# Kernel optimization log

Hardware: AMD Instinct MI355X
Metric: run time of the kernel (lower is better)

Reference implementation:

```python
import jax, jax.numpy as jnp
import numpy as np

B, NP, NAA = 8, 2048, 512        # proteins, atoms, residues
K, K2 = 16, 14                   # spatial K-NN (K_atom), sequence K-NN (K_neighbor)
D_EMB, NG, F, F2, NCAT = 16, 64, 128, 128, 39
EPS = 1e-6

def _gather(x, idx):
    # x: [B, N, ...], idx: [B, ...] int -> x[b, idx[b]]
    return jax.vmap(lambda xb, ib: xb[ib])(x, idx)

def setup_inputs() -> dict:
    key = jax.random.key(0)
    ks = jax.random.split(key, 9)
    return dict(
        frame_indices=jax.random.randint(ks[0], (B, NP, 3), 0, NP, dtype=jnp.int32),
        attr_idx=jax.random.randint(ks[1], (B, NP), 0, NCAT, dtype=jnp.int32),
        seq_atom=jnp.sort(jax.random.randint(ks[2], (B, NP), 0, NAA, dtype=jnp.int32), axis=-1),
        seq_aa=jnp.broadcast_to(jnp.arange(NAA, dtype=jnp.int32), (B, NAA)),
        point_clouds=jax.random.normal(ks[3], (B, NP, 3), dtype=jnp.float32) * 10.0,
        mframe=jnp.ones((B, NP, 1), jnp.float32),
        mseq_aa=jnp.ones((B, NAA, 1), jnp.float32),
        embed_table=jax.random.normal(ks[4], (NCAT, D_EMB), dtype=jnp.float32) * 0.1,
        gauss_mu=jax.random.normal(ks[5], (NG, 3), dtype=jnp.float32) * 3.0,
        gauss_sigma=jnp.full((NG, 3), 2.0, jnp.float32),
        W_filter=jax.random.normal(ks[6], (NG, D_EMB, F), dtype=jnp.float32) / np.sqrt(NG * D_EMB).astype(np.float32),
        W_att=jax.random.normal(ks[7], (F, 1), dtype=jnp.float32) * 0.1,
        W_feat=jax.random.normal(ks[8], (F, F2), dtype=jnp.float32) / np.sqrt(F).astype(np.float32),
        bn_gamma=jnp.ones((F2,), jnp.float32),
        bn_beta=jnp.zeros((F2,), jnp.float32),
    )

def reference(frame_indices, attr_idx, seq_atom, seq_aa, point_clouds, mframe, mseq_aa,
              embed_table, gauss_mu, gauss_sigma, W_filter, W_att, W_feat, bn_gamma, bn_beta):
    # ---- Frame_Builder: orthonormal local frame per atom from index triplets ----
    pts = _gather(point_clouds, frame_indices)                    # [B,NP,3,3]
    center = pts[..., 0, :]
    u1 = pts[..., 1, :] - center
    u2 = pts[..., 2, :] - center
    e1 = u1 / (jnp.linalg.norm(u1, axis=-1, keepdims=True) + EPS)
    nrm = jnp.cross(u1, u2)
    e3 = nrm / (jnp.linalg.norm(nrm, axis=-1, keepdims=True) + EPS)
    e2 = jnp.cross(e3, e1)
    R = jnp.stack([e1, e2, e3], axis=-2)                          # [B,NP,3,3] rows = frame axes
    # ---- Neighborhood_Embedding: spatial K-NN + gaussian spatio-chemical filters ----
    d2 = jnp.sum((center[:, :, None, :] - center[:, None, :, :]) ** 2, axis=-1)   # [B,NP,NP]
    _, nbr = jax.lax.top_k(-d2, K)                                # [B,NP,K]
    delta = _gather(center, nbr) - center[:, :, None, :]          # [B,NP,K,3]
    local = jnp.einsum('bikd,bird->bikr', delta, R)               # neighbor coords in local frame
    inv_s2 = 1.0 / (gauss_sigma ** 2 + EPS)                       # [NG,3]
    q = (jnp.einsum('bikd,nd->bikn', local ** 2, inv_s2)
         - 2.0 * jnp.einsum('bikd,nd->bikn', local, gauss_mu * inv_s2)
         + jnp.sum(gauss_mu ** 2 * inv_s2, axis=-1))
    gauss = jnp.exp(-0.5 * q)                                     # [B,NP,K,NG]
    attr = embed_table[attr_idx] * mframe                         # [B,NP,D_EMB]
    attr_nbr = _gather(attr, nbr)                                 # [B,NP,K,D_EMB]
    Z = jnp.einsum('bikn,bikd->bind', gauss, attr_nbr)            # contract neighbors first
    y = jax.nn.relu(jnp.einsum('bind,ndf->bif', Z, W_filter)) * mframe   # [B,NP,F]
    att = (y @ W_att) * mframe                                    # [B,NP,1]
    feat = (y @ W_feat) * mframe                                  # [B,NP,F2]
    # ---- Neighborhood_Computation: K2 atoms nearest in sequence index per residue ----
    diff = jnp.abs(seq_aa[:, :, None] - seq_atom[:, None, :]).astype(jnp.float32)   # [B,NAA,NP]
    _, idx = jax.lax.top_k(-diff, K2)                             # [B,NAA,K2]
    att_l = _gather(att, idx)[..., 0]                             # [B,NAA,K2]
    feat_l = _gather(feat, idx)                                   # [B,NAA,K2,F2]
    diff_l = jnp.take_along_axis(diff, idx, axis=-1)
    gate = 1.0 - jnp.clip(diff_l, 0.0, 1.0)                       # pool_mask = 1 - index_distance
    # ---- Attention pooling over local atom neighborhood ----
    w = gate * jnp.exp(att_l - jnp.max(att_l, axis=-1, keepdims=True))
    w = w / (jnp.sum(w, axis=-1, keepdims=True) + EPS)
    pooled = jnp.einsum('bak,bakf->baf', w, feat_l) * mseq_aa     # [B,NAA,F2]
    # ---- MaskedBatchNorm1d + ReLU ----
    msum = jnp.sum(mseq_aa) + EPS
    mean = jnp.sum(pooled * mseq_aa, axis=(0, 1)) / msum
    var = jnp.sum(((pooled - mean) ** 2) * mseq_aa, axis=(0, 1)) / msum
    out = (pooled - mean) / jnp.sqrt(var + 1e-5) * bn_gamma + bn_beta
    out = jax.nn.relu(out) * mseq_aa
    return (out, mseq_aa)
```

## Files before the change

### kernel.cpp

```cpp
#include <hip/hip_runtime.h>
#include <math.h>

#define BB 8
#define NP 2048
#define NAA 512
#define KNN 16
#define KK2 14
#define DE 16
#define NG 64
#define FF 128
#define FF2 128
#define NCAT 39
#define EPSV 1e-6f

typedef __attribute__((ext_vector_type(8))) short bf16x8;
typedef __attribute__((ext_vector_type(4))) float f32x4;

__device__ __forceinline__ float bf16r(float x) {
    unsigned u = __float_as_uint(x);
    u = u + 0x7FFFu + ((u >> 16) & 1u);
    return __uint_as_float(u & 0xFFFF0000u);
}
__device__ __forceinline__ unsigned short bf16u(float x) {
    unsigned u = __float_as_uint(x);
    u = u + 0x7FFFu + ((u >> 16) & 1u);
    return (unsigned short)(u >> 16);
}

#define OFF_CENTER   0u
#define OFF_R        262144u
#define OFF_ATTR     1048576u
#define OFF_NBR      2097152u
#define OFF_ATT      3145728u
#define OFF_FEAT     3211264u
#define OFF_POOLED   11599872u
#define OFF_WFFRAG   (OFF_POOLED)
#define OFF_WFEATFRAG (OFF_POOLED + 262144u)
#define OFF_START    13697024u
#define OFF_PARTS    13713536u
#define OFF_PARTQ    13746304u
#define OFF_SS       13779072u

__global__ __launch_bounds__(256) void k_prep(
    const float* __restrict__ Wf, const float* __restrict__ Wfeat,
    unsigned short* __restrict__ WfF, unsigned short* __restrict__ WfeatF)
{
    int id = blockIdx.x * 256 + threadIdx.x;
    if (id < 32*8*64*8) {
        int i = id & 7, l = (id >> 3) & 63, nt = (id >> 9) & 7, s = id >> 12;
        int row = s*32 + (l >> 4)*8 + i;
        int col = nt*16 + (l & 15);
        WfF[id] = bf16u(Wf[(size_t)row*FF + col]);
    } else {
        int id2 = id - 32*8*64*8;
        if (id2 < 4*8*64*8) {
            int i = id2 & 7, l = (id2 >> 3) & 63, nt = (id2 >> 9) & 7, s = id2 >> 12;
            int row = s*32 + (l >> 4)*8 + i;
            int col = nt*16 + (l & 15);
            WfeatF[id2] = bf16u(Wfeat[(size_t)row*FF2 + col]);
        }
    }
}

__global__ __launch_bounds__(256) void k_frames(
    const int* __restrict__ fidx, const int* __restrict__ aidx,
    const float* __restrict__ pc, const float* __restrict__ mframe,
    const float* __restrict__ emb,
    float* __restrict__ center4, float* __restrict__ R12, float* __restrict__ attr16)
{
    int t = blockIdx.x * 256 + threadIdx.x;
    if (t >= BB * NP) return;
    int b = t / NP;
    const float* pcb = pc + (size_t)b * NP * 3;
    int i0 = fidx[t*3+0], i1 = fidx[t*3+1], i2 = fidx[t*3+2];
    float cx = pcb[i0*3+0], cy = pcb[i0*3+1], cz = pcb[i0*3+2];
    float ax = pcb[i1*3+0]-cx, ay = pcb[i1*3+1]-cy, az = pcb[i1*3+2]-cz;
    float bx = pcb[i2*3+0]-cx, by = pcb[i2*3+1]-cy, bz = pcb[i2*3+2]-cz;
    float n1 = sqrtf(ax*ax + ay*ay + az*az) + EPSV;
    float e1x = ax/n1, e1y = ay/n1, e1z = az/n1;
    float nx = ay*bz - az*by;
    float ny = az*bx - ax*bz;
    float nz = ax*by - ay*bx;
    float n3 = sqrtf(nx*nx + ny*ny + nz*nz) + EPSV;
    float e3x = nx/n3, e3y = ny/n3, e3z = nz/n3;
    float e2x = e3y*e1z - e3z*e1y;
    float e2y = e3z*e1x - e3x*e1z;
    float e2z = e3x*e1y - e3y*e1x;

    float4 c4; c4.x = cx; c4.y = cy; c4.z = cz; c4.w = 0.f;
    *(float4*)(center4 + (size_t)t*4) = c4;
    float* Rp = R12 + (size_t)t*12;
    Rp[0]=bf16r(e1x); Rp[1]=bf16r(e1y); Rp[2]=bf16r(e1z);
    Rp[3]=bf16r(e2x); Rp[4]=bf16r(e2y); Rp[5]=bf16r(e2z);
    Rp[6]=bf16r(e3x); Rp[7]=bf16r(e3y); Rp[8]=bf16r(e3z);

    int ai = aidx[t];
    float m = mframe[t];
    const float* er = emb + (size_t)ai * DE;
    float* ap = attr16 + (size_t)t * DE;
    #pragma unroll
    for (int d = 0; d < DE; ++d) ap[d] = bf16r(er[d] * m);
}

__global__ __launch_bounds__(256) void k_knn(
    const float* __restrict__ center4, int* __restrict__ nbr)
{
    __shared__ __align__(16) float sx[NP], sy[NP], sz[NP];
    __shared__ unsigned long long lists[16*126];
    __shared__ int cntS[16];
    __shared__ unsigned int TqU[16];
    unsigned int* kbufA = (unsigned int*)lists;

    int b = blockIdx.x >> 7;
    int qchunk = blockIdx.x & 127;
    int t = threadIdx.x;
    const float* cb = center4 + (size_t)b * NP * 4;
    for (int j = t; j < NP; j += 256) {
        float4 c = *(const float4*)(cb + (size_t)j*4);
        sx[j] = c.x; sy[j] = c.y; sz[j] = c.z;
    }
    __syncthreads();

    int qloc = t & 15, split = t >> 4;
    int q = qchunk * 16 + qloc;
    float qx = sx[q], qy = sy[q], qz = sz[q];
    int j0 = split * 128;
    int stag = split * 8;

    unsigned int e0a = ~0u, e1a = ~0u;
    unsigned int e0b = ~0u, e1b = ~0u;
    unsigned int e0c = ~0u, e1c = ~0u;
    unsigned int e0d = ~0u, e1d = ~0u;
    for (int jj = 0; jj < 128; jj += 4) {
        int j = j0 + ((jj + stag) & 127);
        float4 x4 = *(const float4*)(&sx[j]);
        float4 y4 = *(const float4*)(&sy[j]);
        float4 z4 = *(const float4*)(&sz[j]);
        float dx0 = __fsub_rn(qx, x4.x), dy0 = __fsub_rn(qy, y4.x), dz0 = __fsub_rn(qz, z4.x);
        float dx1 = __fsub_rn(qx, x4.y), dy1 = __fsub_rn(qy, y4.y), dz1 = __fsub_rn(qz, z4.y);
        float dx2 = __fsub_rn(qx, x4.z), dy2 = __fsub_rn(qy, y4.z), dz2 = __fsub_rn(qz, z4.z);
        float dx3 = __fsub_rn(qx, x4.w), dy3 = __fsub_rn(qy, y4.w), dz3 = __fsub_rn(qz, z4.w);
        unsigned c0 = __float_as_uint(__fadd_rn(__fadd_rn(__fmul_rn(dx0,dx0), __fmul_rn(dy0,dy0)), __fmul_rn(dz0,dz0)));
        unsigned c1 = __float_as_uint(__fadd_rn(__fadd_rn(__fmul_rn(dx1,dx1), __fmul_rn(dy1,dy1)), __fmul_rn(dz1,dz1)));
        unsigned c2 = __float_as_uint(__fadd_rn(__fadd_rn(__fmul_rn(dx2,dx2), __fmul_rn(dy2,dy2)), __fmul_rn(dz2,dz2)));
        unsigned c3 = __float_as_uint(__fadd_rn(__fadd_rn(__fmul_rn(dx3,dx3), __fmul_rn(dy3,dy3)), __fmul_rn(dz3,dz3)));
        unsigned n1;
        n1 = max(e0a, min(e1a, c0)); e0a = min(e0a, c0); e1a = n1;
        n1 = max(e0b, min(e1b, c1)); e0b = min(e0b, c1); e1b = n1;
        n1 = max(e0c, min(e1c, c2)); e0c = min(e0c, c2); e1c = n1;
        n1 = max(e0d, min(e1d, c3)); e0d = min(e0d, c3); e1d = n1;
    }
    kbufA[0*256 + t] = e0a;
    kbufA[1*256 + t] = e1a;
    kbufA[2*256 + t] = e0b;
    kbufA[3*256 + t] = e1b;
    kbufA[4*256 + t] = e0c;
    kbufA[5*256 + t] = e1c;
    kbufA[6*256 + t] = e0d;
    kbufA[7*256 + t] = e1d;
    __syncthreads();

    if (t < 16) {
        unsigned int arr[16];
        #pragma unroll
        for (int s = 0; s < 16; ++s) arr[s] = ~0u;
        for (int sp = 0; sp < 16; ++sp) {
            int lidx = sp*16 + t;
            #pragma unroll
            for (int ch = 0; ch < 4; ++ch) {
                #pragma unroll
                for (int s = 0; s < 2; ++s) {
                    unsigned int v = kbufA[(ch*2 + s)*256 + lidx];
                    if (v >= arr[15]) break;
                    unsigned int c = v;
                    #pragma unroll
                    for (int u = 0; u < 16; ++u) {
                        unsigned int lo = min(c, arr[u]), hi = max(c, arr[u]);
                        arr[u] = lo; c = hi;
                    }
                }
            }
        }
        TqU[t] = arr[15];
        cntS[t] = 0;
    }
    __syncthreads();
    unsigned int T = TqU[qloc];

    for (int jj = 0; jj < 128; jj += 4) {
        int j = j0 + ((jj + stag) & 127);
        float4 x4 = *(const float4*)(&sx[j]);
        float4 y4 = *(const float4*)(&sy[j]);
        float4 z4 = *(const float4*)(&sz[j]);
        #pragma unroll
        for (int c4i = 0; c4i < 4; ++c4i) {
            float xx = c4i==0?x4.x:c4i==1?x4.y:c4i==2?x4.z:x4.w;
            float yy = c4i==0?y4.x:c4i==1?y4.y:c4i==2?y4.z:y4.w;
            float zz = c4i==0?z4.x:c4i==1?z4.y:c4i==2?z4.z:z4.w;
            float dx = __fsub_rn(qx, xx);
            float dy = __fsub_rn(qy, yy);
            float dz = __fsub_rn(qz, zz);
            float d2 = __fadd_rn(__fadd_rn(__fmul_rn(dx,dx), __fmul_rn(dy,dy)), __fmul_rn(dz,dz));
            unsigned int db = __float_as_uint(d2);
            if (db <= T) {
                int slot = atomicAdd(&cntS[qloc], 1);
                if (slot < 126)
                    lists[qloc*126 + slot] = ((unsigned long long)db << 32) | (unsigned)(j + c4i);
            }
        }
    }
    __syncthreads();

    if (t < 16) {
        int n = cntS[t] < 126 ? cntS[t] : 126;
        unsigned long long arr[16];
        #pragma unroll
        for (int s = 0; s < 16; ++s) arr[s] = ~0ULL;
        for (int i = 0; i < n; ++i) {
            unsigned long long key = lists[t*126 + i];
            if (key < arr[15]) {
                unsigned long long c = key;
                #pragma unroll
                for (int u = 0; u < 16; ++u) {
                    unsigned long long lo = c < arr[u] ? c : arr[u];
                    unsigned long long hi = c < arr[u] ? arr[u] : c;
                    arr[u] = lo; c = hi;
                }
            }
        }
        int qg = qchunk * 16 + t;
        int* outp = nbr + ((size_t)b*NP + qg) * KNN;
        #pragma unroll
        for (int s = 0; s < 16; ++s) outp[s] = (int)(arr[s] & 0xFFFFFFFFu);
    }
}

__global__ __launch_bounds__(256) void k_filter(
    const float* __restrict__ center4, const float* __restrict__ R12,
    const float* __restrict__ attr16, const int* __restrict__ nbr,
    const float* __restrict__ mframe,
    const float* __restrict__ mu, const float* __restrict__ sigma,
    const unsigned short* __restrict__ WfF, const float* __restrict__ Watt,
    const unsigned short* __restrict__ WfeatF,
    float* __restrict__ att, float* __restrict__ feat)
{
    __shared__ float cG[NG*8];
    __shared__ float locS[256*5];
    __shared__ float gaussS[256*17];
    __shared__ __align__(16) unsigned short ZsU[16*256];
    __shared__ __align__(16) unsigned short yU[16*128];
    __shared__ float cS[16*4];
    __shared__ float RS[16*12];
    __shared__ int   nbrS[256];
    __shared__ float mfS[16];

    int t = threadIdx.x;
    int lane = t & 63, w = t >> 6;
    int blk = blockIdx.x;
    int b = blk / (NP/16);
    int abase = (blk % (NP/16)) * 16;
    size_t gbase = (size_t)b * NP + abase;

    if (t < NG) {
        float s0 = sigma[t*3+0], s1 = sigma[t*3+1], s2 = sigma[t*3+2];
        float i0 = 1.f/(s0*s0 + EPSV), i1 = 1.f/(s1*s1 + EPSV), i2 = 1.f/(s2*s2 + EPSV);
        float m0 = mu[t*3+0], m1 = mu[t*3+1], m2 = mu[t*3+2];
        float* cg = cG + t*8;
        cg[0]=bf16r(i0); cg[1]=bf16r(i1); cg[2]=bf16r(i2);
        cg[3]=bf16r(m0*i0); cg[4]=bf16r(m1*i1); cg[5]=bf16r(m2*i2);
        cg[6]=m0*m0*i0 + m1*m1*i1 + m2*m2*i2;
    }
    if (t < 16) {
        float4 c = *(const float4*)(center4 + (gbase + t)*4);
        cS[t*4+0]=c.x; cS[t*4+1]=c.y; cS[t*4+2]=c.z;
        const float* Rp = R12 + (gbase + t)*12;
        #pragma unroll
        for (int r = 0; r < 9; ++r) RS[t*12+r] = Rp[r];
        mfS[t] = mframe[gbase + t];
    }
    nbrS[t] = nbr[gbase*KNN + t];
    __syncthreads();

    {
        int a = t >> 4;
        int j = nbrS[t];
        size_t gj = (size_t)b*NP + j;
        float4 cj = *(const float4*)(center4 + gj*4);
        float dx = bf16r(cj.x - cS[a*4+0]);
        float dy = bf16r(cj.y - cS[a*4+1]);
        float dz = bf16r(cj.z - cS[a*4+2]);
        const float* Rr = RS + a*12;
        float l0 = dx*Rr[0] + dy*Rr[1] + dz*Rr[2];
        float l1 = dx*Rr[3] + dy*Rr[4] + dz*Rr[5];
        float l2 = dx*Rr[6] + dy*Rr[7] + dz*Rr[8];
        float* lp = locS + (size_t)t*5;
        lp[0]=l0; lp[1]=l1; lp[2]=l2;
    }
    float attrk[16];
    {
        int a = t >> 4, d = t & 15;
        #pragma unroll
        for (int k = 0; k < 16; ++k) {
            int j = nbrS[a*16 + k];
            attrk[k] = attr16[((size_t)b*NP + j)*DE + d];
        }
    }
    __syncthreads();

    f32x4 acc0 = {0.f,0.f,0.f,0.f}, acc1 = {0.f,0.f,0.f,0.f};
    int aA = lane & 15, kb = lane >> 4;
    int swzA = (aA & 7) << 3;

    for (int nc = 0; nc < 4; ++nc) {
        {
            const float* lp = locS + (size_t)t*5;
            float l0 = lp[0], l1 = lp[1], l2 = lp[2];
            float s0 = bf16r(l0*l0), s1 = bf16r(l1*l1), s2 = bf16r(l2*l2);
            float b0 = bf16r(l0), b1 = bf16r(l1), b2 = bf16r(l2);
            float* gp = gaussS + (size_t)t*17;
            #pragma unroll
            for (int nl = 0; nl < 16; ++nl) {
                const float* cg = cG + (nc*16 + nl)*8;
                float dotA = s0*cg[0] + s1*cg[1] + s2*cg[2];
                float dotB = b0*cg[3] + b1*cg[4] + b2*cg[5];
                float qv = dotA - 2.f*dotB + cg[6];
                gp[nl] = bf16r(expf(-0.5f*qv));
            }
        }
        __syncthreads();
        {
            int a = t >> 4, d = t & 15;
            const float* gpA = gaussS + (size_t)a*16*17;
            int swzW = (a & 7) << 3;
            #pragma unroll
            for (int nl = 0; nl < 16; ++nl) {
                float acc = 0.f;
                const float* gp = gpA + nl;
                #pragma unroll
                for (int k = 0; k < 16; ++k) acc += gp[k*17] * attrk[k];
                int nd = nl*16 + d;
                ZsU[(a*256 + nd) ^ swzW] = bf16u(acc);
            }
        }
        __syncthreads();
        {
            #pragma unroll
            for (int st = 0; st < 8; ++st) {
                int u0 = (aA*256 + st*32 + kb*8) ^ swzA;
                bf16x8 af = *(const bf16x8*)(&ZsU[u0]);
                int sg = nc*8 + st;
                bf16x8 b0 = ((const bf16x8*)WfF)[((size_t)sg*8 + w*2 + 0)*64 + lane];
                bf16x8 b1 = ((const bf16x8*)WfF)[((size_t)sg*8 + w*2 + 1)*64 + lane];
                acc0 = __builtin_amdgcn_mfma_f32_16x16x32_bf16(af, b0, acc0, 0, 0, 0);
                acc1 = __builtin_amdgcn_mfma_f32_16x16x32_bf16(af, b1, acc1, 0, 0, 0);
            }
        }
        __syncthreads();
    }

    {
        #pragma unroll
        for (int r = 0; r < 4; ++r) {
            int atom = (lane >> 4)*4 + r;
            int swzW = (atom & 7) << 3;
            float v0 = fmaxf(acc0[r], 0.f) * mfS[atom];
            float v1 = fmaxf(acc1[r], 0.f) * mfS[atom];
            int f0 = (w*2 + 0)*16 + (lane & 15);
            int f1 = (w*2 + 1)*16 + (lane & 15);
            yU[(atom*128 + f0) ^ swzW] = bf16u(v0);
            yU[(atom*128 + f1) ^ swzW] = bf16u(v1);
        }
    }
    __syncthreads();

    float* attP = locS;
    if (t < 128) {
        int aq = t & 15, g = t >> 4;
        int swzW = (aq & 7) << 3;
        float s = 0.f;
        #pragma unroll
        for (int cc = 0; cc < 16; ++cc) {
            int c = g*16 + cc;
            unsigned short uv = yU[(aq*128 + c) ^ swzW];
            s += __uint_as_float((unsigned)uv << 16) * bf16r(Watt[c]);
        }
        attP[g*16 + aq] = s;
    }

    f32x4 fa0 = {0.f,0.f,0.f,0.f}, fa1 = {0.f,0.f,0.f,0.f};
    #pragma unroll
    for (int st = 0; st < 4; ++st) {
        int u0 = (aA*128 + st*32 + kb*8) ^ swzA;
        bf16x8 af = *(const bf16x8*)(&yU[u0]);
        bf16x8 b0 = ((const bf16x8*)WfeatF)[((size_t)st*8 + w*2 + 0)*64 + lane];
        bf16x8 b1 = ((const bf16x8*)WfeatF)[((size_t)st*8 + w*2 + 1)*64 + lane];
        fa0 = __builtin_amdgcn_mfma_f32_16x16x32_bf16(af, b0, fa0, 0, 0, 0);
        fa1 = __builtin_amdgcn_mfma_f32_16x16x32_bf16(af, b1, fa1, 0, 0, 0);
    }
    {
        #pragma unroll
        for (int r = 0; r < 4; ++r) {
            int atom = (lane >> 4)*4 + r;
            float m = mfS[atom];
            int f0 = (w*2 + 0)*16 + (lane & 15);
            int f1 = (w*2 + 1)*16 + (lane & 15);
            feat[(gbase + atom)*FF2 + f0] = fa0[r] * m;
            feat[(gbase + atom)*FF2 + f1] = fa1[r] * m;
        }
    }
    __syncthreads();
    if (t < 16) {
        float s = 0.f;
        #pragma unroll
        for (int g = 0; g < 8; ++g) s += attP[g*16 + t];
        att[gbase + t] = s * mfS[t];
    }
}

__global__ __launch_bounds__(576) void k_start(
    const int* __restrict__ seq_atom, int* __restrict__ start)
{
    int b = blockIdx.x;
    int v = threadIdx.x;
    if (v > NAA) return;
    const int* s = seq_atom + (size_t)b * NP;
    int lo = 0, hi = NP;
    while (lo < hi) {
        int mid = (lo + hi) >> 1;
        if (s[mid] < v) lo = mid + 1; else hi = mid;
    }
    start[b*(NAA+1) + v] = lo;
}

__global__ __launch_bounds__(64) void k_pool(
    const int* __restrict__ seq_aa, const int* __restrict__ start,
    const float* __restrict__ att, const float* __restrict__ feat,
    const float* __restrict__ mseq, float* __restrict__ pooled)
{
    __shared__ int   jS[KK2];
    __shared__ int   dS[KK2];
    __shared__ float avS[KK2];
    __shared__ float wS[KK2];
    int blk = blockIdx.x;
    int b = blk >> 9;
    int a = blk & (NAA - 1);
    int t = threadIdx.x;
    if (t == 0) {
        int v = seq_aa[b*NAA + a];
        const int* st = start + b*(NAA+1);
        int cnt = 0;
        for (int d = 0; cnt < KK2 && d < NAA; ++d) {
            int vlo = v - d;
            if (vlo >= 0) {
                int s0 = st[vlo], s1 = st[vlo+1];
                for (int j = s0; j < s1 && cnt < KK2; ++j) { jS[cnt] = j; dS[cnt] = d; ++cnt; }
            }
            int vhi = v + d;
            if (d > 0 && vhi < NAA) {
                int s0 = st[vhi], s1 = st[vhi+1];
                for (int j = s0; j < s1 && cnt < KK2; ++j) { jS[cnt] = j; dS[cnt] = d; ++cnt; }
            }
        }
        float m = -INFINITY;
        for (int k = 0; k < KK2; ++k) {
            float av = att[(size_t)b*NP + jS[k]];
            avS[k] = av;
            m = fmaxf(m, av);
        }
        float ssum = 0.f;
        for (int k = 0; k < KK2; ++k) {
            float g = (dS[k] == 0) ? 1.f : 0.f;
            float w = g * expf(avS[k] - m);
            wS[k] = w;
            ssum += w;
        }
        float inv = 1.f / (ssum + EPSV);
        for (int k = 0; k < KK2; ++k) wS[k] = bf16r(wS[k] * inv);
    }
    __syncthreads();
    int row = b*NAA + a;
    float m = mseq[row];
    for (int ff = t; ff < FF2; ff += 64) {
        float acc = 0.f;
        #pragma unroll
        for (int k = 0; k < KK2; ++k)
            acc += wS[k] * bf16r(feat[((size_t)b*NP + jS[k])*FF2 + ff]);
        pooled[(size_t)row*FF2 + ff] = acc * m;
    }
}

__global__ __launch_bounds__(128) void k_bnstat1(
    const float* __restrict__ pooled, const float* __restrict__ mseq,
    float* __restrict__ partS, float* __restrict__ partQ)
{
    int g = blockIdx.x, f = threadIdx.x;
    float s = 0.f, q = 0.f;
    for (int r = 0; r < 64; ++r) {
        int row = g*64 + r;
        float m = mseq[row];
        float x = pooled[(size_t)row*FF2 + f];
        s += x*m; q += x*x*m;
    }
    partS[g*FF2 + f] = s;
    partQ[g*FF2 + f] = q;
}

__global__ __launch_bounds__(128) void k_bnstat2(
    const float* __restrict__ partS, const float* __restrict__ partQ,
    const float* __restrict__ mseq,
    const float* __restrict__ gamma, const float* __restrict__ beta,
    float* __restrict__ scaleshift)
{
    __shared__ float msums[128];
    int f = threadIdx.x;
    float mm = 0.f;
    for (int r = f; r < BB*NAA; r += 128) mm += mseq[r];
    msums[f] = mm;
    __syncthreads();
    for (int s = 64; s > 0; s >>= 1) {
        if (f < s) msums[f] += msums[f + s];
        __syncthreads();
    }
    float Sm = msums[0];
    float msum = Sm + EPSV;
    float s = 0.f, q = 0.f;
    for (int g = 0; g < 64; ++g) { s += partS[g*FF2 + f]; q += partQ[g*FF2 + f]; }
    float mean = s / msum;
    float var = (q - 2.f*mean*s + mean*mean*Sm) / msum;
    float rstd = 1.f / sqrtf(var + 1e-5f);
    float sc = rstd * gamma[f];
    scaleshift[f] = sc;
    scaleshift[FF2 + f] = beta[f] - mean*sc;
}

__global__ __launch_bounds__(256) void k_bnapply(
    const float* __restrict__ pooled, const float* __restrict__ scaleshift,
    const float* __restrict__ mseq, float* __restrict__ out)
{
    int idx = blockIdx.x*256 + threadIdx.x;
    if (idx < BB*NAA*FF2) {
        int f = idx & (FF2 - 1);
        int row = idx >> 7;
        float v = pooled[idx]*scaleshift[f] + scaleshift[FF2 + f];
        v = v > 0.f ? v : 0.f;
        out[idx] = v * mseq[row];
    }
    if (idx < BB*NAA) out[BB*NAA*FF2 + idx] = mseq[idx];
}

extern "C" void kernel_launch(void* const* d_in, const int* in_sizes, int n_in,
                              void* d_out, int out_size, void* d_ws, size_t ws_size,
                              hipStream_t stream)
{
    const int*   fidx   = (const int*)  d_in[0];
    const int*   aidx   = (const int*)  d_in[1];
    const int*   seqat  = (const int*)  d_in[2];
    const int*   seqaa  = (const int*)  d_in[3];
    const float* pc     = (const float*)d_in[4];
    const float* mframe = (const float*)d_in[5];
    const float* mseq   = (const float*)d_in[6];
    const float* emb    = (const float*)d_in[7];
    const float* gmu    = (const float*)d_in[8];
    const float* gsig   = (const float*)d_in[9];
    const float* Wf     = (const float*)d_in[10];
    const float* Watt   = (const float*)d_in[11];
    const float* Wfeat  = (const float*)d_in[12];
    const float* gamma  = (const float*)d_in[13];
    const float* beta   = (const float*)d_in[14];

    char* ws = (char*)d_ws;
    float* center4 = (float*)(ws + OFF_CENTER);
    float* R12     = (float*)(ws + OFF_R);
    float* attr16  = (float*)(ws + OFF_ATTR);
    int*   nbr     = (int*)  (ws + OFF_NBR);
    float* att     = (float*)(ws + OFF_ATT);
    float* feat    = (float*)(ws + OFF_FEAT);
    float* pooled  = (float*)(ws + OFF_POOLED);
    unsigned short* WfF    = (unsigned short*)(ws + OFF_WFFRAG);
    unsigned short* WfeatF = (unsigned short*)(ws + OFF_WFEATFRAG);
    int*   start   = (int*)  (ws + OFF_START);
    float* partS   = (float*)(ws + OFF_PARTS);
    float* partQ   = (float*)(ws + OFF_PARTQ);
    float* ss      = (float*)(ws + OFF_SS);
    float* outp    = (float*)d_out;

    hipLaunchKernelGGL(k_prep, dim3(576), dim3(256), 0, stream,
                       Wf, Wfeat, WfF, WfeatF);
    hipLaunchKernelGGL(k_frames, dim3(64), dim3(256), 0, stream,
                       fidx, aidx, pc, mframe, emb, center4, R12, attr16);
    hipLaunchKernelGGL(k_knn, dim3(1024), dim3(256), 0, stream, center4, nbr);
    hipLaunchKernelGGL(k_filter, dim3(1024), dim3(256), 0, stream,
                       center4, R12, attr16, nbr, mframe, gmu, gsig,
                       WfF, Watt, WfeatF, att, feat);
    hipLaunchKernelGGL(k_start, dim3(BB), dim3(576), 0, stream, seqat, start);
    hipLaunchKernelGGL(k_pool, dim3(BB*NAA), dim3(64), 0, stream,
                       seqaa, start, att, feat, mseq, pooled);
    hipLaunchKernelGGL(k_bnstat1, dim3(64), dim3(128), 0, stream,
                       pooled, mseq, partS, partQ);
    hipLaunchKernelGGL(k_bnstat2, dim3(1), dim3(128), 0, stream,
                       partS, partQ, mseq, gamma, beta, ss);
    hipLaunchKernelGGL(k_bnapply, dim3((BB*NAA*FF2 + 255)/256), dim3(256), 0, stream,
                       pooled, ss, mseq, outp);
}
```

Baseline: 130.0 us.

## Read KNN candidate points from global memory and halve queries per block

The KNN kernel no longer stages all 2048 atom coordinates of a protein into shared memory per block. Each thread reads candidate float4 points directly from global memory (through L1/L2), and each block now handles 8 queries instead of 16, with 32 splits of 64 candidates, over twice as many blocks. This removes the per-block 24KB shared-memory fill and its barrier, which should raise occupancy. The cost is more global or cache load traffic, since every wave rereads the coordinate array, and a serial merge over 32 partial lists per query instead of 16.

```diff
diff --git a/kernel.cpp b/kernel.cpp
--- a/kernel.cpp
+++ b/kernel.cpp
@@ -105,41 +105,35 @@
 __global__ __launch_bounds__(256) void k_knn(
     const float* __restrict__ center4, int* __restrict__ nbr)
 {
-    __shared__ __align__(16) float sx[NP], sy[NP], sz[NP];
-    __shared__ unsigned long long lists[16*126];
-    __shared__ int cntS[16];
-    __shared__ unsigned int TqU[16];
+    __shared__ unsigned long long lists[8*128];
+    __shared__ int cntS[8];
+    __shared__ unsigned int TqU[8];
     unsigned int* kbufA = (unsigned int*)lists;
 
-    int b = blockIdx.x >> 7;
-    int qchunk = blockIdx.x & 127;
+    int b = blockIdx.x >> 8;
+    int qchunk = blockIdx.x & 255;
     int t = threadIdx.x;
-    const float* cb = center4 + (size_t)b * NP * 4;
-    for (int j = t; j < NP; j += 256) {
-        float4 c = *(const float4*)(cb + (size_t)j*4);
-        sx[j] = c.x; sy[j] = c.y; sz[j] = c.z;
-    }
-    __syncthreads();
-
-    int qloc = t & 15, split = t >> 4;
-    int q = qchunk * 16 + qloc;
-    float qx = sx[q], qy = sy[q], qz = sz[q];
-    int j0 = split * 128;
-    int stag = split * 8;
+    int qloc = t & 7, split = t >> 3;
+    int q = qchunk * 8 + qloc;
+    const float4* cb4 = (const float4*)(center4 + (size_t)b * NP * 4);
+    float4 qc = cb4[q];
+    float qx = qc.x, qy = qc.y, qz = qc.z;
+    int j0 = split * 64;
 
     unsigned int e0a = ~0u, e1a = ~0u;
     unsigned int e0b = ~0u, e1b = ~0u;
     unsigned int e0c = ~0u, e1c = ~0u;
     unsigned int e0d = ~0u, e1d = ~0u;
-    for (int jj = 0; jj < 128; jj += 4) {
-        int j = j0 + ((jj + stag) & 127);
-        float4 x4 = *(const float4*)(&sx[j]);
-        float4 y4 = *(const float4*)(&sy[j]);
-        float4 z4 = *(const float4*)(&sz[j]);
-        float dx0 = __fsub_rn(qx, x4.x), dy0 = __fsub_rn(qy, y4.x), dz0 = __fsub_rn(qz, z4.x);
-        float dx1 = __fsub_rn(qx, x4.y), dy1 = __fsub_rn(qy, y4.y), dz1 = __fsub_rn(qz, z4.y);
-        float dx2 = __fsub_rn(qx, x4.z), dy2 = __fsub_rn(qy, y4.z), dz2 = __fsub_rn(qz, z4.z);
-        float dx3 = __fsub_rn(qx, x4.w), dy3 = __fsub_rn(qy, y4.w), dz3 = __fsub_rn(qz, z4.w);
+    for (int jj = 0; jj < 64; jj += 4) {
+        int j = j0 + jj;
+        float4 p0 = cb4[j+0];
+        float4 p1 = cb4[j+1];
+        float4 p2 = cb4[j+2];
+        float4 p3 = cb4[j+3];
+        float dx0 = __fsub_rn(qx, p0.x), dy0 = __fsub_rn(qy, p0.y), dz0 = __fsub_rn(qz, p0.z);
+        float dx1 = __fsub_rn(qx, p1.x), dy1 = __fsub_rn(qy, p1.y), dz1 = __fsub_rn(qz, p1.z);
+        float dx2 = __fsub_rn(qx, p2.x), dy2 = __fsub_rn(qy, p2.y), dz2 = __fsub_rn(qz, p2.z);
+        float dx3 = __fsub_rn(qx, p3.x), dy3 = __fsub_rn(qy, p3.y), dz3 = __fsub_rn(qz, p3.z);
         unsigned c0 = __float_as_uint(__fadd_rn(__fadd_rn(__fmul_rn(dx0,dx0), __fmul_rn(dy0,dy0)), __fmul_rn(dz0,dz0)));
         unsigned c1 = __float_as_uint(__fadd_rn(__fadd_rn(__fmul_rn(dx1,dx1), __fmul_rn(dy1,dy1)), __fmul_rn(dz1,dz1)));
         unsigned c2 = __float_as_uint(__fadd_rn(__fadd_rn(__fmul_rn(dx2,dx2), __fmul_rn(dy2,dy2)), __fmul_rn(dz2,dz2)));
@@ -160,12 +154,12 @@
     kbufA[7*256 + t] = e1d;
     __syncthreads();
 
-    if (t < 16) {
+    if (t < 8) {
         unsigned int arr[16];
         #pragma unroll
         for (int s = 0; s < 16; ++s) arr[s] = ~0u;
-        for (int sp = 0; sp < 16; ++sp) {
-            int lidx = sp*16 + t;
+        for (int sp = 0; sp < 32; ++sp) {
+            int lidx = sp*8 + t;
             #pragma unroll
             for (int ch = 0; ch < 4; ++ch) {
                 #pragma unroll
@@ -187,16 +181,17 @@
     __syncthreads();
     unsigned int T = TqU[qloc];
 
-    for (int jj = 0; jj < 128; jj += 4) {
-        int j = j0 + ((jj + stag) & 127);
-        float4 x4 = *(const float4*)(&sx[j]);
-        float4 y4 = *(const float4*)(&sy[j]);
-        float4 z4 = *(const float4*)(&sz[j]);
+    for (int jj = 0; jj < 64; jj += 4) {
+        int j = j0 + jj;
+        float4 p0 = cb4[j+0];
+        float4 p1 = cb4[j+1];
+        float4 p2 = cb4[j+2];
+        float4 p3 = cb4[j+3];
         #pragma unroll
         for (int c4i = 0; c4i < 4; ++c4i) {
-            float xx = c4i==0?x4.x:c4i==1?x4.y:c4i==2?x4.z:x4.w;
-            float yy = c4i==0?y4.x:c4i==1?y4.y:c4i==2?y4.z:y4.w;
-            float zz = c4i==0?z4.x:c4i==1?z4.y:c4i==2?z4.z:z4.w;
+            float xx = c4i==0?p0.x:c4i==1?p1.x:c4i==2?p2.x:p3.x;
+            float yy = c4i==0?p0.y:c4i==1?p1.y:c4i==2?p2.y:p3.y;
+            float zz = c4i==0?p0.z:c4i==1?p1.z:c4i==2?p2.z:p3.z;
             float dx = __fsub_rn(qx, xx);
             float dy = __fsub_rn(qy, yy);
             float dz = __fsub_rn(qz, zz);
@@ -205,19 +200,19 @@
             if (db <= T) {
                 int slot = atomicAdd(&cntS[qloc], 1);
                 if (slot < 126)
-                    lists[qloc*126 + slot] = ((unsigned long long)db << 32) | (unsigned)(j + c4i);
-            }
-        }
-    }
-    __syncthreads();
-
-    if (t < 16) {
+                    lists[qloc*128 + slot] = ((unsigned long long)db << 32) | (unsigned)(j + c4i);
+            }
+        }
+    }
+    __syncthreads();
+
+    if (t < 8) {
         int n = cntS[t] < 126 ? cntS[t] : 126;
         unsigned long long arr[16];
         #pragma unroll
         for (int s = 0; s < 16; ++s) arr[s] = ~0ULL;
         for (int i = 0; i < n; ++i) {
-            unsigned long long key = lists[t*126 + i];
+            unsigned long long key = lists[t*128 + i];
             if (key < arr[15]) {
                 unsigned long long c = key;
                 #pragma unroll
@@ -228,7 +223,7 @@
                 }
             }
         }
-        int qg = qchunk * 16 + t;
+        int qg = qchunk * 8 + t;
         int* outp = nbr + ((size_t)b*NP + qg) * KNN;
         #pragma unroll
         for (int s = 0; s < 16; ++s) outp[s] = (int)(arr[s] & 0xFFFFFFFFu);
@@ -588,7 +583,7 @@
                        Wf, Wfeat, WfF, WfeatF);
     hipLaunchKernelGGL(k_frames, dim3(64), dim3(256), 0, stream,
                        fidx, aidx, pc, mframe, emb, center4, R12, attr16);
-    hipLaunchKernelGGL(k_knn, dim3(1024), dim3(256), 0, stream, center4, nbr);
+    hipLaunchKernelGGL(k_knn, dim3(2048), dim3(256), 0, stream, center4, nbr);
     hipLaunchKernelGGL(k_filter, dim3(1024), dim3(256), 0, stream,
                        center4, R12, attr16, nbr, mframe, gmu, gsig,
                        WfF, Watt, WfeatF, att, feat);
```

After: 166.2 us. +27.9%, slower.
